# Performance work log

Hardware: AMD Instinct MI355X
Metric: run time of the kernel (lower is better)

Reference implementation:

```python
import jax, jax.numpy as jnp
import numpy as np

N_NODES = 50000
N_EDGES = 800000
D = 128
N_LAYERS = 3
EPS = 1e-5  # torch LayerNorm default


def _gcn_conv(x, src, dst, dinv, W, b):
    # PyG GCNConv: h = x @ W; out[i] = sum_{(s->i)} dinv[s]*dinv[i]*h[s] + dinv[i]^2*h[i] + b
    h = x @ W
    norm = dinv[src] * dinv[dst]                      # [E]
    msgs = h[src] * norm[:, None]                     # [E, D] gather
    agg = jax.ops.segment_sum(msgs, dst, num_segments=N_NODES)  # scatter-add
    agg = agg + h * (dinv * dinv)[:, None]            # self-loop term
    return agg + b


def _layer_norm(x, gamma, beta):
    mu = jnp.mean(x, axis=-1, keepdims=True)
    var = jnp.mean(jnp.square(x - mu), axis=-1, keepdims=True)
    return (x - mu) * jax.lax.rsqrt(var + EPS) * gamma + beta


def setup_inputs() -> dict:
    key = jax.random.key(0)
    ks = jax.random.split(key, 4)
    x = jax.random.normal(ks[0], (N_NODES, D), dtype=jnp.float32)
    edge_index = jax.random.randint(ks[1], (2, N_EDGES), 0, N_NODES, dtype=jnp.int64)
    Ws = jax.random.normal(ks[2], (N_LAYERS, D, D), dtype=jnp.float32) * (1.0 / np.sqrt(D))
    bs = jnp.zeros((N_LAYERS, D), dtype=jnp.float32)
    gammas = jnp.ones((N_LAYERS, D), dtype=jnp.float32)
    betas = jnp.zeros((N_LAYERS, D), dtype=jnp.float32)
    return {"x": x, "edge_index": edge_index, "Ws": Ws, "bs": bs,
            "gammas": gammas, "betas": betas}


def reference(x, edge_index, Ws, bs, gammas, betas):
    src, dst = edge_index[0], edge_index[1]
    # GCN symmetric normalization with self-loops: deg[i] = in-degree(i) + 1
    deg = jnp.zeros((N_NODES,), dtype=x.dtype).at[dst].add(1.0) + 1.0
    dinv = jax.lax.rsqrt(deg)
    h = x
    for i in range(N_LAYERS):
        x_new = _gcn_conv(h, src, dst, dinv, Ws[i], bs[i])
        x_new = _layer_norm(x_new, gammas[i], betas[i])
        x_new = jax.nn.relu(x_new)  # dropout is identity in eval mode
        h = h + x_new if i > 0 else x_new
    return h
```

## Files before the change

kernel.cpp:

```cpp
#include <hip/hip_runtime.h>
#include <hip/hip_bf16.h>

#define NN 50000
#define NE 800000
#define DD 128
#define NB 196
#define NCH 8
#define CHSZ 6250
#define NC2 (NN * NCH)
#define NSB 391
#define PH (64 * NB)
#define FS 2048
#define NSL 391
#define HB 3125
#define CB 3125
#define WB 192
#define LN_EPS 1e-5f

typedef __bf16 bf16x8 __attribute__((ext_vector_type(8)));
typedef float f32x4 __attribute__((ext_vector_type(4)));

__device__ inline ushort f2bf_bits(float f) {
    union { __hip_bfloat16 h; ushort u; } c;
    c.h = __float2bfloat16(f);
    return c.u;
}

__global__ void hist_cast_kernel(const int* __restrict__ src, const int* __restrict__ dst,
                                 int* __restrict__ counts2, const float* __restrict__ x,
                                 uint4* __restrict__ fb0, const float* __restrict__ W,
                                 ushort* __restrict__ Wt) {
    int b = blockIdx.x;
    if (b < HB) {
        int e = b * 256 + threadIdx.x;
        int s = src[e], d = dst[e];
        atomicAdd(&counts2[d * NCH + s / CHSZ], 1);
    } else if (b < HB + CB) {
        int i = (b - HB) * 256 + threadIdx.x;
        float4 v0 = ((const float4*)x)[2 * i];
        float4 v1 = ((const float4*)x)[2 * i + 1];
        union { ushort us[8]; uint4 u; } pk;
        pk.us[0] = f2bf_bits(v0.x); pk.us[1] = f2bf_bits(v0.y);
        pk.us[2] = f2bf_bits(v0.z); pk.us[3] = f2bf_bits(v0.w);
        pk.us[4] = f2bf_bits(v1.x); pk.us[5] = f2bf_bits(v1.y);
        pk.us[6] = f2bf_bits(v1.z); pk.us[7] = f2bf_bits(v1.w);
        fb0[i] = pk.u;
    } else {
        int i = (b - HB - CB) * 256 + threadIdx.x;
        int l = i >> 14, k = (i >> 7) & 127, n = i & 127;
        Wt[l * 16384 + n * 128 + k] = f2bf_bits(W[i]);
    }
}

__global__ __launch_bounds__(1024) void scan1024_blocks(int* __restrict__ data,
                                                        int* __restrict__ bsums) {
    __shared__ int ws[16];
    int gid = blockIdx.x * 1024 + threadIdx.x;
    int lane = threadIdx.x & 63, wid = threadIdx.x >> 6;
    int v = (gid < NC2) ? data[gid] : 0;
    int x = v;
#pragma unroll
    for (int off = 1; off < 64; off <<= 1) {
        int t = __shfl_up(x, off, 64);
        if (lane >= off) x += t;
    }
    if (lane == 63) ws[wid] = x;
    __syncthreads();
    if (threadIdx.x == 0) {
        int run = 0;
        for (int i = 0; i < 16; ++i) { int t = ws[i]; ws[i] = run; run += t; }
        bsums[blockIdx.x] = run;
    }
    __syncthreads();
    if (gid < NC2) data[gid] = x - v + ws[wid];
}

__global__ __launch_bounds__(1024) void scan_sums1024(int* __restrict__ bsums, int nb) {
    __shared__ int ws[16];
    int tid = threadIdx.x;
    int lane = tid & 63, wid = tid >> 6;
    int v = (tid < nb) ? bsums[tid] : 0;
    int x = v;
#pragma unroll
    for (int off = 1; off < 64; off <<= 1) {
        int t = __shfl_up(x, off, 64);
        if (lane >= off) x += t;
    }
    if (lane == 63) ws[wid] = x;
    __syncthreads();
    if (tid == 0) {
        int run = 0;
        for (int i = 0; i < 16; ++i) { int t = ws[i]; ws[i] = run; run += t; }
    }
    __syncthreads();
    if (tid < nb) bsums[tid] = x - v + ws[wid];
}

__global__ void finalize_kernel(const int* __restrict__ excl2, const int* __restrict__ bsums,
                                int* __restrict__ row_ptr, int* __restrict__ next_pos2,
                                float* __restrict__ dinv, int* __restrict__ degarr,
                                int* __restrict__ bh) {
    __shared__ int lh[64];
    if (threadIdx.x < 64) lh[threadIdx.x] = 0;
    __syncthreads();
    int d = blockIdx.x * 256 + threadIdx.x;
    if (d < NN) {
        int base = d * NCH;
        int p0 = excl2[base] + bsums[base >> 10];
#pragma unroll
        for (int c = 0; c < NCH; ++c) {
            int idx = base + c;
            next_pos2[idx] = excl2[idx] + bsums[idx >> 10];
        }
        int nxt = (d == NN - 1) ? NE : excl2[base + NCH] + bsums[(base + NCH) >> 10];
        int deg = nxt - p0;
        row_ptr[d] = p0;
        dinv[d] = rsqrtf((float)deg + 1.0f);
        degarr[d] = deg;
        atomicAdd(&lh[min(deg, 63)], 1);
    }
    __syncthreads();
    if (threadIdx.x < 64) bh[threadIdx.x * NB + blockIdx.x] = lh[threadIdx.x];
    if (blockIdx.x == 0 && threadIdx.x == 0) row_ptr[NN] = NE;
}

__global__ __launch_bounds__(1024) void permscan_kernel(int* __restrict__ bh) {
    __shared__ int wsum[16];
    const int CH = 13;
    int tid = threadIdx.x;
    int base = tid * CH;
    int vals[CH];
    int s = 0;
#pragma unroll
    for (int i = 0; i < CH; ++i) {
        int idx = base + i;
        int v = (idx < PH) ? bh[idx] : 0;
        vals[i] = s;
        s += v;
    }
    int lane = tid & 63, wid = tid >> 6;
    int x = s;
#pragma unroll
    for (int off = 1; off < 64; off <<= 1) {
        int t = __shfl_up(x, off, 64);
        if (lane >= off) x += t;
    }
    if (lane == 63) wsum[wid] = x;
    __syncthreads();
    if (tid == 0) {
        int run = 0;
        for (int i = 0; i < 16; ++i) { int t = wsum[i]; wsum[i] = run; run += t; }
    }
    __syncthreads();
    int texcl = x - s + wsum[wid];
#pragma unroll
    for (int i = 0; i < CH; ++i) {
        int idx = base + i;
        if (idx < PH) bh[idx] = texcl + vals[i];
    }
}

__global__ void permscatter_kernel(const int* __restrict__ degarr, const int* __restrict__ bh,
                                   int* __restrict__ perm) {
    __shared__ int lh[64];
    __shared__ int lbase[64];
    if (threadIdx.x < 64) {
        lh[threadIdx.x] = 0;
        lbase[threadIdx.x] = bh[threadIdx.x * NB + blockIdx.x];
    }
    __syncthreads();
    int gid = blockIdx.x * 256 + threadIdx.x;
    if (gid < NN) {
        int b = min(degarr[gid], 63);
        int r = atomicAdd(&lh[b], 1);
        perm[lbase[b] + r] = gid;
    }
}

__global__ void fill_kernel(const int* __restrict__ src, const int* __restrict__ dst,
                            int* __restrict__ next_pos2, const float* __restrict__ dinv,
                            int2* __restrict__ edge2) {
    int slice = blockIdx.x >> 3;
    int r = blockIdx.x & 7;
    int base = slice * FS;
#pragma unroll 2
    for (int i = threadIdx.x; i < FS; i += 256) {
        int e = base + i;
        if (e < NE) {
            int d = dst[e];
            if (d / CHSZ == r) {
                int s = src[e];
                int pos = atomicAdd(&next_pos2[d * NCH + s / CHSZ], 1);
                int2 o;
                o.x = s;
                o.y = __float_as_int(dinv[s] * dinv[d]);
                edge2[pos] = o;
            }
        }
    }
}

template <bool RES, bool FINAL>
__global__ __launch_bounds__(256) void layer_kernel(
    const ushort* __restrict__ fin, const int* __restrict__ row_ptr,
    const int2* __restrict__ edge2, const int* __restrict__ perm,
    const float* __restrict__ dinv, const ushort* __restrict__ Wt,
    const float* __restrict__ bias, const float* __restrict__ gamma,
    const float* __restrict__ beta, ushort* __restrict__ fout, float* __restrict__ out) {
    __shared__ uint4 sA[16 * 17];
    __shared__ int sNode[16];
    __shared__ float sLN1[4][16], sLN2[4][16];

    int w = threadIdx.x >> 6, lane = threadIdx.x & 63;
    int g = lane >> 4, t = lane & 15;
    int arow = w * 4 + g;
    int slot = blockIdx.x * 16 + arow;
    int node = perm[slot];
    if (t == 0) sNode[arow] = node;

    {
        int beg = row_ptr[node], end = row_ptr[node + 1];
        const uint4* cu4 = (const uint4*)fin;
        float acc[8] = {};
        int e = beg;
        for (; e + 4 <= end; e += 4) {
            int2 a0 = edge2[e + 0];
            int2 a1 = edge2[e + 1];
            int2 a2 = edge2[e + 2];
            int2 a3 = edge2[e + 3];
            uint4 v0 = cu4[a0.x * 16 + t];
            uint4 v1 = cu4[a1.x * 16 + t];
            uint4 v2 = cu4[a2.x * 16 + t];
            uint4 v3 = cu4[a3.x * 16 + t];
            uint vv0[4] = {v0.x, v0.y, v0.z, v0.w};
            uint vv1[4] = {v1.x, v1.y, v1.z, v1.w};
            uint vv2[4] = {v2.x, v2.y, v2.z, v2.w};
            uint vv3[4] = {v3.x, v3.y, v3.z, v3.w};
            float w0 = __int_as_float(a0.y), w1 = __int_as_float(a1.y);
            float w2 = __int_as_float(a2.y), w3 = __int_as_float(a3.y);
#pragma unroll
            for (int i = 0; i < 4; ++i) {
                acc[2 * i] = fmaf(w0, __uint_as_float(vv0[i] << 16), acc[2 * i]);
                acc[2 * i + 1] = fmaf(w0, __uint_as_float(vv0[i] & 0xffff0000u), acc[2 * i + 1]);
                acc[2 * i] = fmaf(w1, __uint_as_float(vv1[i] << 16), acc[2 * i]);
                acc[2 * i + 1] = fmaf(w1, __uint_as_float(vv1[i] & 0xffff0000u), acc[2 * i + 1]);
                acc[2 * i] = fmaf(w2, __uint_as_float(vv2[i] << 16), acc[2 * i]);
                acc[2 * i + 1] = fmaf(w2, __uint_as_float(vv2[i] & 0xffff0000u), acc[2 * i + 1]);
                acc[2 * i] = fmaf(w3, __uint_as_float(vv3[i] << 16), acc[2 * i]);
                acc[2 * i + 1] = fmaf(w3, __uint_as_float(vv3[i] & 0xffff0000u), acc[2 * i + 1]);
            }
        }
        for (; e < end; ++e) {
            int2 a = edge2[e];
            uint4 v = cu4[a.x * 16 + t];
            uint vv[4] = {v.x, v.y, v.z, v.w};
            float ww = __int_as_float(a.y);
#pragma unroll
            for (int i = 0; i < 4; ++i) {
                acc[2 * i] = fmaf(ww, __uint_as_float(vv[i] << 16), acc[2 * i]);
                acc[2 * i + 1] = fmaf(ww, __uint_as_float(vv[i] & 0xffff0000u), acc[2 * i + 1]);
            }
        }
        float di = dinv[node];
        float w2s = di * di;
        {
            uint4 v = cu4[node * 16 + t];
            uint vv[4] = {v.x, v.y, v.z, v.w};
#pragma unroll
            for (int i = 0; i < 4; ++i) {
                acc[2 * i] = fmaf(w2s, __uint_as_float(vv[i] << 16), acc[2 * i]);
                acc[2 * i + 1] = fmaf(w2s, __uint_as_float(vv[i] & 0xffff0000u), acc[2 * i + 1]);
            }
        }
        union { ushort us[8]; uint4 u; } pk;
#pragma unroll
        for (int i = 0; i < 8; ++i) pk.us[i] = f2bf_bits(acc[i]);
        sA[arow * 17 + t] = pk.u;
    }
    __syncthreads();

    int q = lane >> 4, m = lane & 15;
    f32x4 c0 = (f32x4){0.f, 0.f, 0.f, 0.f};
    f32x4 c1 = (f32x4){0.f, 0.f, 0.f, 0.f};
    int n0 = 16 * (2 * w), n1 = 16 * (2 * w + 1);
#pragma unroll
    for (int kk = 0; kk < 4; ++kk) {
        bf16x8 af = *(const bf16x8*)&sA[m * 17 + kk * 4 + q];
        bf16x8 b0 = *(const bf16x8*)(Wt + (n0 + m) * DD + kk * 32 + q * 8);
        bf16x8 b1 = *(const bf16x8*)(Wt + (n1 + m) * DD + kk * 32 + q * 8);
        c0 = __builtin_amdgcn_mfma_f32_16x16x32_bf16(af, b0, c0, 0, 0, 0);
        c1 = __builtin_amdgcn_mfma_f32_16x16x32_bf16(af, b1, c1, 0, 0, 0);
    }

    float bb0 = bias[n0 + m], bb1 = bias[n1 + m];
    float s1[4], s2[4];
#pragma unroll
    for (int r = 0; r < 4; ++r) {
        float v0 = c0[r] + bb0, v1 = c1[r] + bb1;
        c0[r] = v0; c1[r] = v1;
        s1[r] = v0 + v1;
        s2[r] = v0 * v0 + v1 * v1;
    }
#pragma unroll
    for (int off = 1; off <= 8; off <<= 1) {
#pragma unroll
        for (int r = 0; r < 4; ++r) {
            s1[r] += __shfl_xor(s1[r], off, 64);
            s2[r] += __shfl_xor(s2[r], off, 64);
        }
    }
    if (m == 0) {
#pragma unroll
        for (int r = 0; r < 4; ++r) {
            sLN1[w][q * 4 + r] = s1[r];
            sLN2[w][q * 4 + r] = s2[r];
        }
    }
    __syncthreads();
    float ga0 = gamma[n0 + m], ga1 = gamma[n1 + m];
    float be0 = beta[n0 + m], be1 = beta[n1 + m];
#pragma unroll
    for (int r = 0; r < 4; ++r) {
        int row = q * 4 + r;
        float S1 = sLN1[0][row] + sLN1[1][row] + sLN1[2][row] + sLN1[3][row];
        float S2 = sLN2[0][row] + sLN2[1][row] + sLN2[2][row] + sLN2[3][row];
        float mu = S1 * (1.f / 128.f);
        float var = S2 * (1.f / 128.f) - mu * mu;
        float rstd = rsqrtf(var + LN_EPS);
        int nd = sNode[row];
        size_t rb = (size_t)nd * DD;
        float o0 = fmaxf((c0[r] - mu) * rstd * ga0 + be0, 0.f);
        float o1 = fmaxf((c1[r] - mu) * rstd * ga1 + be1, 0.f);
        if (RES) {
            o0 += __uint_as_float(((uint)fin[rb + n0 + m]) << 16);
            o1 += __uint_as_float(((uint)fin[rb + n1 + m]) << 16);
        }
        if (FINAL) {
            out[rb + n0 + m] = o0;
            out[rb + n1 + m] = o1;
        } else {
            fout[rb + n0 + m] = f2bf_bits(o0);
            fout[rb + n1 + m] = f2bf_bits(o1);
        }
    }
}


extern "C" void kernel_launch(void* const* d_in, const int* in_sizes, int n_in,
                              void* d_out, int out_size, void* d_ws, size_t ws_size,
                              hipStream_t stream) {
    const float* x = (const float*)d_in[0];
    const int* edge = (const int*)d_in[1];
    const float* Ws = (const float*)d_in[2];
    const float* bs = (const float*)d_in[3];
    const float* gs = (const float*)d_in[4];
    const float* bes = (const float*)d_in[5];
    float* out = (float*)d_out;
    const int* src = edge;
    const int* dst = edge + NE;

    char* p = (char*)d_ws;
    int* counts2 = (int*)p;     p += (size_t)NC2 * 4;
    int* bsums = (int*)p;       p += 1024 * 4;
    int* row_ptr = (int*)p;     p += (size_t)(NN + 4) * 4;
    int* next_pos2 = (int*)p;   p += (size_t)NC2 * 4;
    float* dinv = (float*)p;    p += (size_t)NN * 4;
    int* degarr = (int*)p;      p += (size_t)NN * 4;
    int* bh = (int*)p;          p += (size_t)PH * 4;
    int* perm = (int*)p;        p += (size_t)NN * 4;
    int2* edge2 = (int2*)p;     p += (size_t)NE * 8;
    ushort* fb0 = (ushort*)p;   p += (size_t)NN * DD * 2;
    ushort* fb1 = (ushort*)p;   p += (size_t)NN * DD * 2;
    ushort* Wt = (ushort*)p;    p += (size_t)3 * DD * DD * 2;

    hipMemsetAsync(counts2, 0, (size_t)NC2 * 4, stream);
    hist_cast_kernel<<<HB + CB + WB, 256, 0, stream>>>(src, dst, counts2, x, (uint4*)fb0, Ws,
                                                       Wt);
    scan1024_blocks<<<NSB, 1024, 0, stream>>>(counts2, bsums);
    scan_sums1024<<<1, 1024, 0, stream>>>(bsums, NSB);
    finalize_kernel<<<NB, 256, 0, stream>>>(counts2, bsums, row_ptr, next_pos2, dinv, degarr,
                                            bh);
    permscan_kernel<<<1, 1024, 0, stream>>>(bh);
    permscatter_kernel<<<NB, 256, 0, stream>>>(degarr, bh, perm);
    fill_kernel<<<NSL * 8, 256, 0, stream>>>(src, dst, next_pos2, dinv, edge2);

    int lg = NN / 16;
    layer_kernel<false, false><<<lg, 256, 0, stream>>>(
        fb0, row_ptr, edge2, perm, dinv, Wt, bs, gs, bes, fb1, out);
    layer_kernel<true, false><<<lg, 256, 0, stream>>>(
        fb1, row_ptr, edge2, perm, dinv, Wt + 16384, bs + DD, gs + DD, bes + DD, fb0, out);
    layer_kernel<true, true><<<lg, 256, 0, stream>>>(
        fb0, row_ptr, edge2, perm, dinv, Wt + 32768, bs + 2 * DD, gs + 2 * DD, bes + 2 * DD,
        fb1, out);
}
```

Baseline: 312.9 us.

## Walk gather edges in source-chunk phases with block-level sync and slice prefetch

Edges are already sorted by source chunk within each destination row. The gather loop now runs chunk by chunk using per-chunk row pointers (rp2), with a __syncthreads after each chunk. This keeps every block in the same 1.6MB source slice of the feature buffer at the same time, so the working set stays in L2. Each block also touches part of the next slice ahead of time as a software prefetch, kept alive by a dummy xor and a conditional store. The costs are eight block barriers per node group, a smaller unroll (2 instead of 4), an extra 1.6MB row-pointer array, and stalls for blocks whose rows are uneven across chunks.

```diff
diff --git a/kernel.cpp b/kernel.cpp
--- a/kernel.cpp
+++ b/kernel.cpp
@@ -15,6 +15,8 @@
 #define HB 3125
 #define CB 3125
 #define WB 192
+#define SLICE_BYTES 1600000
+#define SLICE_LINES 25600
 #define LN_EPS 1e-5f
 
 typedef __bf16 bf16x8 __attribute__((ext_vector_type(8)));
@@ -98,8 +100,8 @@
 
 __global__ void finalize_kernel(const int* __restrict__ excl2, const int* __restrict__ bsums,
                                 int* __restrict__ row_ptr, int* __restrict__ next_pos2,
-                                float* __restrict__ dinv, int* __restrict__ degarr,
-                                int* __restrict__ bh) {
+                                int* __restrict__ rp2, float* __restrict__ dinv,
+                                int* __restrict__ degarr, int* __restrict__ bh) {
     __shared__ int lh[64];
     if (threadIdx.x < 64) lh[threadIdx.x] = 0;
     __syncthreads();
@@ -110,7 +112,9 @@
 #pragma unroll
         for (int c = 0; c < NCH; ++c) {
             int idx = base + c;
-            next_pos2[idx] = excl2[idx] + bsums[idx >> 10];
+            int v = excl2[idx] + bsums[idx >> 10];
+            next_pos2[idx] = v;
+            rp2[idx] = v;
         }
         int nxt = (d == NN - 1) ? NE : excl2[base + NCH] + bsums[(base + NCH) >> 10];
         int deg = nxt - p0;
@@ -203,10 +207,11 @@
 template <bool RES, bool FINAL>
 __global__ __launch_bounds__(256) void layer_kernel(
     const ushort* __restrict__ fin, const int* __restrict__ row_ptr,
-    const int2* __restrict__ edge2, const int* __restrict__ perm,
-    const float* __restrict__ dinv, const ushort* __restrict__ Wt,
-    const float* __restrict__ bias, const float* __restrict__ gamma,
-    const float* __restrict__ beta, ushort* __restrict__ fout, float* __restrict__ out) {
+    const int* __restrict__ rp2, const int2* __restrict__ edge2,
+    const int* __restrict__ perm, const float* __restrict__ dinv,
+    const ushort* __restrict__ Wt, const float* __restrict__ bias,
+    const float* __restrict__ gamma, const float* __restrict__ beta,
+    ushort* __restrict__ fout, float* __restrict__ out, int* __restrict__ scratch) {
     __shared__ uint4 sA[16 * 17];
     __shared__ int sNode[16];
     __shared__ float sLN1[4][16], sLN2[4][16];
@@ -218,39 +223,40 @@
     int node = perm[slot];
     if (t == 0) sNode[arow] = node;
 
-    {
-        int beg = row_ptr[node], end = row_ptr[node + 1];
-        const uint4* cu4 = (const uint4*)fin;
-        float acc[8] = {};
-        int e = beg;
-        for (; e + 4 <= end; e += 4) {
+    const char* fc = (const char*)fin;
+    int pfline = (blockIdx.x >> 3) * 68 + threadIdx.x;
+    bool dopf = (threadIdx.x < 68) && (pfline < SLICE_LINES);
+    uint pfs = 0;
+    if (dopf) pfs ^= *(const uint*)(fc + (size_t)pfline * 64);
+
+    int base2 = node * NCH;
+    int endrow = row_ptr[node + 1];
+    const uint4* cu4 = (const uint4*)fin;
+    float acc[8] = {};
+#pragma unroll 1
+    for (int c = 0; c < NCH; ++c) {
+        uint va = 0;
+        if (c + 1 < NCH && dopf)
+            va = *(const uint*)(fc + (size_t)(c + 1) * SLICE_BYTES + (size_t)pfline * 64);
+        int e = rp2[base2 + c];
+        int segend = (c + 1 < NCH) ? rp2[base2 + c + 1] : endrow;
+        for (; e + 2 <= segend; e += 2) {
             int2 a0 = edge2[e + 0];
             int2 a1 = edge2[e + 1];
-            int2 a2 = edge2[e + 2];
-            int2 a3 = edge2[e + 3];
             uint4 v0 = cu4[a0.x * 16 + t];
             uint4 v1 = cu4[a1.x * 16 + t];
-            uint4 v2 = cu4[a2.x * 16 + t];
-            uint4 v3 = cu4[a3.x * 16 + t];
             uint vv0[4] = {v0.x, v0.y, v0.z, v0.w};
             uint vv1[4] = {v1.x, v1.y, v1.z, v1.w};
-            uint vv2[4] = {v2.x, v2.y, v2.z, v2.w};
-            uint vv3[4] = {v3.x, v3.y, v3.z, v3.w};
             float w0 = __int_as_float(a0.y), w1 = __int_as_float(a1.y);
-            float w2 = __int_as_float(a2.y), w3 = __int_as_float(a3.y);
 #pragma unroll
             for (int i = 0; i < 4; ++i) {
                 acc[2 * i] = fmaf(w0, __uint_as_float(vv0[i] << 16), acc[2 * i]);
                 acc[2 * i + 1] = fmaf(w0, __uint_as_float(vv0[i] & 0xffff0000u), acc[2 * i + 1]);
                 acc[2 * i] = fmaf(w1, __uint_as_float(vv1[i] << 16), acc[2 * i]);
                 acc[2 * i + 1] = fmaf(w1, __uint_as_float(vv1[i] & 0xffff0000u), acc[2 * i + 1]);
-                acc[2 * i] = fmaf(w2, __uint_as_float(vv2[i] << 16), acc[2 * i]);
-                acc[2 * i + 1] = fmaf(w2, __uint_as_float(vv2[i] & 0xffff0000u), acc[2 * i + 1]);
-                acc[2 * i] = fmaf(w3, __uint_as_float(vv3[i] << 16), acc[2 * i]);
-                acc[2 * i + 1] = fmaf(w3, __uint_as_float(vv3[i] & 0xffff0000u), acc[2 * i + 1]);
             }
         }
-        for (; e < end; ++e) {
+        if (e < segend) {
             int2 a = edge2[e];
             uint4 v = cu4[a.x * 16 + t];
             uint vv[4] = {v.x, v.y, v.z, v.w};
@@ -261,16 +267,18 @@
                 acc[2 * i + 1] = fmaf(ww, __uint_as_float(vv[i] & 0xffff0000u), acc[2 * i + 1]);
             }
         }
+        pfs ^= va;
+        __syncthreads();
+    }
+    {
         float di = dinv[node];
         float w2s = di * di;
-        {
-            uint4 v = cu4[node * 16 + t];
-            uint vv[4] = {v.x, v.y, v.z, v.w};
-#pragma unroll
-            for (int i = 0; i < 4; ++i) {
-                acc[2 * i] = fmaf(w2s, __uint_as_float(vv[i] << 16), acc[2 * i]);
-                acc[2 * i + 1] = fmaf(w2s, __uint_as_float(vv[i] & 0xffff0000u), acc[2 * i + 1]);
-            }
+        uint4 v = cu4[node * 16 + t];
+        uint vv[4] = {v.x, v.y, v.z, v.w};
+#pragma unroll
+        for (int i = 0; i < 4; ++i) {
+            acc[2 * i] = fmaf(w2s, __uint_as_float(vv[i] << 16), acc[2 * i]);
+            acc[2 * i + 1] = fmaf(w2s, __uint_as_float(vv[i] & 0xffff0000u), acc[2 * i + 1]);
         }
         union { ushort us[8]; uint4 u; } pk;
 #pragma unroll
@@ -343,6 +351,7 @@
             fout[rb + n1 + m] = f2bf_bits(o1);
         }
     }
+    if (pfs == 0xDEADBEEFu) *scratch = (int)pfs;
 }
 
 
@@ -364,6 +373,7 @@
     int* bsums = (int*)p;       p += 1024 * 4;
     int* row_ptr = (int*)p;     p += (size_t)(NN + 4) * 4;
     int* next_pos2 = (int*)p;   p += (size_t)NC2 * 4;
+    int* rp2 = (int*)p;         p += (size_t)NC2 * 4;
     float* dinv = (float*)p;    p += (size_t)NN * 4;
     int* degarr = (int*)p;      p += (size_t)NN * 4;
     int* bh = (int*)p;          p += (size_t)PH * 4;
@@ -372,24 +382,26 @@
     ushort* fb0 = (ushort*)p;   p += (size_t)NN * DD * 2;
     ushort* fb1 = (ushort*)p;   p += (size_t)NN * DD * 2;
     ushort* Wt = (ushort*)p;    p += (size_t)3 * DD * DD * 2;
+    int* scratch = bsums + 512;
 
     hipMemsetAsync(counts2, 0, (size_t)NC2 * 4, stream);
     hist_cast_kernel<<<HB + CB + WB, 256, 0, stream>>>(src, dst, counts2, x, (uint4*)fb0, Ws,
                                                        Wt);
     scan1024_blocks<<<NSB, 1024, 0, stream>>>(counts2, bsums);
     scan_sums1024<<<1, 1024, 0, stream>>>(bsums, NSB);
-    finalize_kernel<<<NB, 256, 0, stream>>>(counts2, bsums, row_ptr, next_pos2, dinv, degarr,
-                                            bh);
+    finalize_kernel<<<NB, 256, 0, stream>>>(counts2, bsums, row_ptr, next_pos2, rp2, dinv,
+                                            degarr, bh);
     permscan_kernel<<<1, 1024, 0, stream>>>(bh);
     permscatter_kernel<<<NB, 256, 0, stream>>>(degarr, bh, perm);
     fill_kernel<<<NSL * 8, 256, 0, stream>>>(src, dst, next_pos2, dinv, edge2);
 
     int lg = NN / 16;
     layer_kernel<false, false><<<lg, 256, 0, stream>>>(
-        fb0, row_ptr, edge2, perm, dinv, Wt, bs, gs, bes, fb1, out);
+        fb0, row_ptr, rp2, edge2, perm, dinv, Wt, bs, gs, bes, fb1, out, scratch);
     layer_kernel<true, false><<<lg, 256, 0, stream>>>(
-        fb1, row_ptr, edge2, perm, dinv, Wt + 16384, bs + DD, gs + DD, bes + DD, fb0, out);
+        fb1, row_ptr, rp2, edge2, perm, dinv, Wt + 16384, bs + DD, gs + DD, bes + DD, fb0, out,
+        scratch);
     layer_kernel<true, true><<<lg, 256, 0, stream>>>(
-        fb0, row_ptr, edge2, perm, dinv, Wt + 32768, bs + 2 * DD, gs + 2 * DD, bes + 2 * DD,
-        fb1, out);
-}
+        fb0, row_ptr, rp2, edge2, perm, dinv, Wt + 32768, bs + 2 * DD, gs + 2 * DD,
+        bes + 2 * DD, fb1, out, scratch);
+}
```

New measurement: 382.1 us. 1.22x slower.
